# Kernel optimization log

Hardware: AMD Instinct MI355X
Metric: run time of the kernel (lower is better)

Reference implementation:

```python
import jax, jax.numpy as jnp
import numpy as np

LEN = 16384
TAU = 20.0
DT = 1.0


def setup_inputs() -> dict:
    key = jax.random.key(0)
    k1, k2 = jax.random.split(key)
    inp = jax.random.normal(k1, (1024, 1, LEN), dtype=jnp.float32)
    tgt = jax.random.normal(k2, (1024, 1, LEN), dtype=jnp.float32)
    return {"input": inp, "target": tgt}


def _exp_causal_filter(x, decay):
    # x: [B, 1, L]. Causal exponential filter:
    #   y[t] = sum_{m=0}^{t} x[t-m] * decay**m  ==  y[t] = decay*y[t-1] + x[t]
    # This is exactly conv1d(pad(x, (L-1, 0)), kernel=[exp(-t/tau) for t in L-1..0]).
    def step(carry, xt):
        y = decay * carry + xt
        return y, y

    x_t = jnp.moveaxis(x, -1, 0)  # [L, B, 1]
    y0 = jnp.zeros(x.shape[:-1], x.dtype)  # [B, 1]
    _, ys = jax.lax.scan(step, y0, x_t)  # [L, B, 1]
    return jnp.moveaxis(ys, 0, -1)  # [B, 1, L]


def reference(input, target):
    decay = jnp.exp(jnp.asarray(-DT * 0.0 - 1.0 / TAU, input.dtype))  # exp(-1/tau)
    diff = input - target
    filtered = _exp_causal_filter(diff, decay)
    return jnp.sqrt((1.0 / TAU) * jnp.sum(filtered * filtered) * DT)
```

## Files before the change

### kernel.cpp

```cpp
#include <hip/hip_runtime.h>
#include <math.h>

#define LEN       16384
#define NTHREADS  1024
#define SEG       16
#define NWAVES    16

#define DECAY_F 0.951229424500714f
#define D16_F   0.449328964117222f
#define G16_F   7.5886329f

__device__ __forceinline__ int swz(int a) { return a ^ ((a >> 5) & 31); }

#define STEP(xv) { s = __builtin_fmaf(DECAY_F, s, (xv)); ww *= DECAY_F; \
                   A = __builtin_fmaf(s, s, A); Bc = __builtin_fmaf(ww, s, Bc); }

__global__ __launch_bounds__(NTHREADS) void vr_main(
    const float* __restrict__ in, const float* __restrict__ tgt,
    float* __restrict__ partial)
{
    __shared__ float smem[LEN];
    __shared__ float wa[NWAVES], wb[NWAVES], red[NWAVES];

    const int tid  = threadIdx.x;
    const int lane = tid & 63;
    const int wid  = tid >> 6;
    const long long rb = (long long)blockIdx.x * LEN;
    const float4* __restrict__ in4 = (const float4*)(in  + rb);
    const float4* __restrict__ tg4 = (const float4*)(tgt + rb);

    const int cb4 = (wid << 8) + lane;

    const float4 a0 = in4[cb4];       const float4 b0 = tg4[cb4];
    const float4 a1 = in4[cb4 +  64]; const float4 b1 = tg4[cb4 +  64];
    const float4 a2 = in4[cb4 + 128]; const float4 b2 = tg4[cb4 + 128];
    const float4 a3 = in4[cb4 + 192]; const float4 b3 = tg4[cb4 + 192];
    __builtin_amdgcn_sched_barrier(0);

    {
        int base = cb4 * 4;
        smem[swz(base + 0)] = a0.x - b0.x; smem[swz(base + 1)] = a0.y - b0.y;
        smem[swz(base + 2)] = a0.z - b0.z; smem[swz(base + 3)] = a0.w - b0.w;
        base = (cb4 + 64) * 4;
        smem[swz(base + 0)] = a1.x - b1.x; smem[swz(base + 1)] = a1.y - b1.y;
        smem[swz(base + 2)] = a1.z - b1.z; smem[swz(base + 3)] = a1.w - b1.w;
        base = (cb4 + 128) * 4;
        smem[swz(base + 0)] = a2.x - b2.x; smem[swz(base + 1)] = a2.y - b2.y;
        smem[swz(base + 2)] = a2.z - b2.z; smem[swz(base + 3)] = a2.w - b2.w;
        base = (cb4 + 192) * 4;
        smem[swz(base + 0)] = a3.x - b3.x; smem[swz(base + 1)] = a3.y - b3.y;
        smem[swz(base + 2)] = a3.z - b3.z; smem[swz(base + 3)] = a3.w - b3.w;
    }
    asm volatile("s_waitcnt lgkmcnt(0)" ::: "memory");
    __builtin_amdgcn_sched_barrier(0);

    float s = 0.f, A = 0.f, Bc = 0.f, ww = 1.f;
    const int base = tid * SEG;
    #pragma unroll
    for (int i = 0; i < SEG; ++i) {
        const float x = smem[swz(base + i)];
        STEP(x)
    }

    float a = D16_F;
    float b = s;
    #pragma unroll
    for (int j = 1; j < 64; j <<= 1) {
        const float au = __shfl_up(a, j);
        const float bu = __shfl_up(b, j);
        if (lane >= j) {
            b = __builtin_fmaf(a, bu, b);
            a *= au;
        }
    }
    if (lane == 63) { wa[wid] = a; wb[wid] = b; }
    __syncthreads();

    float C = 0.f;
    for (int k = 0; k < wid; ++k) C = __builtin_fmaf(wa[k], C, wb[k]);
    float aex = __shfl_up(a, 1);
    float bex = __shfl_up(b, 1);
    if (lane == 0) { aex = 1.f; bex = 0.f; }
    const float c = __builtin_fmaf(aex, C, bex);

    float part = A + 2.f * c * Bc + (c * c) * G16_F;

    #pragma unroll
    for (int j = 32; j > 0; j >>= 1) part += __shfl_down(part, j);
    if (lane == 0) red[wid] = part;
    __syncthreads();
    if (tid == 0) {
        float t = 0.f;
        #pragma unroll
        for (int k = 0; k < NWAVES; ++k) t += red[k];
        partial[blockIdx.x] = t;
    }
}

__global__ __launch_bounds__(1024) void vr_final(
    const float* __restrict__ partial, int n, float* __restrict__ out)
{
    __shared__ float red[16];
    const int tid = threadIdx.x;
    float v = 0.f;
    for (int k = tid; k < n; k += 1024) v += partial[k];
    #pragma unroll
    for (int j = 32; j > 0; j >>= 1) v += __shfl_down(v, j);
    const int lane = tid & 63, wid = tid >> 6;
    if (lane == 0) red[wid] = v;
    __syncthreads();
    if (tid == 0) {
        float t = 0.f;
        #pragma unroll
        for (int k = 0; k < 16; ++k) t += red[k];
        out[0] = sqrtf(t * 0.05f);
    }
}

extern "C" void kernel_launch(void* const* d_in, const int* in_sizes, int n_in,
                              void* d_out, int out_size, void* d_ws, size_t ws_size,
                              hipStream_t stream) {
    const float* in  = (const float*)d_in[0];
    const float* tgt = (const float*)d_in[1];
    float* out = (float*)d_out;
    float* ws  = (float*)d_ws;
    const int rows = in_sizes[0] / LEN;

    vr_main<<<dim3(rows), dim3(NTHREADS), 0, stream>>>(in, tgt, ws);
    vr_final<<<dim3(1), dim3(1024), 0, stream>>>(ws, rows, out);
}
```

Baseline: 27.95 us.

## Process two rows per block and prefetch the next row during the scan

Each block now handles two rows instead of one. Global loads for the second row are issued right after the first row's differences go to shared memory, so those loads overlap the first row's scan and reduction. This is meant to hide memory latency and cut per-block launch and reduction overhead. The cost is half as many blocks (512 instead of 1024 on 256 CUs), an extra barrier per row, higher register pressure from the prefetched data, and an assumption that the row count is divisible by two.

```diff
diff --git a/kernel.cpp b/kernel.cpp
--- a/kernel.cpp
+++ b/kernel.cpp
@@ -5,6 +5,7 @@
 #define NTHREADS  1024
 #define SEG       16
 #define NWAVES    16
+#define RPB       2
 
 #define DECAY_F 0.951229424500714f
 #define D16_F   0.449328964117222f
@@ -14,6 +15,10 @@
 
 #define STEP(xv) { s = __builtin_fmaf(DECAY_F, s, (xv)); ww *= DECAY_F; \
                    A = __builtin_fmaf(s, s, A); Bc = __builtin_fmaf(ww, s, Bc); }
+
+#define DSW(base4, A4, B4) { const int _b = (base4) * 4; \
+    smem[swz(_b + 0)] = (A4).x - (B4).x; smem[swz(_b + 1)] = (A4).y - (B4).y; \
+    smem[swz(_b + 2)] = (A4).z - (B4).z; smem[swz(_b + 3)] = (A4).w - (B4).w; }
 
 __global__ __launch_bounds__(NTHREADS) void vr_main(
     const float* __restrict__ in, const float* __restrict__ tgt,
@@ -25,69 +30,76 @@
     const int tid  = threadIdx.x;
     const int lane = tid & 63;
     const int wid  = tid >> 6;
-    const long long rb = (long long)blockIdx.x * LEN;
-    const float4* __restrict__ in4 = (const float4*)(in  + rb);
-    const float4* __restrict__ tg4 = (const float4*)(tgt + rb);
-
     const int cb4 = (wid << 8) + lane;
 
-    const float4 a0 = in4[cb4];       const float4 b0 = tg4[cb4];
-    const float4 a1 = in4[cb4 +  64]; const float4 b1 = tg4[cb4 +  64];
-    const float4 a2 = in4[cb4 + 128]; const float4 b2 = tg4[cb4 + 128];
-    const float4 a3 = in4[cb4 + 192]; const float4 b3 = tg4[cb4 + 192];
-    __builtin_amdgcn_sched_barrier(0);
+    const long long row0 = (long long)blockIdx.x * RPB;
+    const float4* __restrict__ in4 = (const float4*)(in  + row0 * LEN);
+    const float4* __restrict__ tg4 = (const float4*)(tgt + row0 * LEN);
 
-    {
-        int base = cb4 * 4;
-        smem[swz(base + 0)] = a0.x - b0.x; smem[swz(base + 1)] = a0.y - b0.y;
-        smem[swz(base + 2)] = a0.z - b0.z; smem[swz(base + 3)] = a0.w - b0.w;
-        base = (cb4 + 64) * 4;
-        smem[swz(base + 0)] = a1.x - b1.x; smem[swz(base + 1)] = a1.y - b1.y;
-        smem[swz(base + 2)] = a1.z - b1.z; smem[swz(base + 3)] = a1.w - b1.w;
-        base = (cb4 + 128) * 4;
-        smem[swz(base + 0)] = a2.x - b2.x; smem[swz(base + 1)] = a2.y - b2.y;
-        smem[swz(base + 2)] = a2.z - b2.z; smem[swz(base + 3)] = a2.w - b2.w;
-        base = (cb4 + 192) * 4;
-        smem[swz(base + 0)] = a3.x - b3.x; smem[swz(base + 1)] = a3.y - b3.y;
-        smem[swz(base + 2)] = a3.z - b3.z; smem[swz(base + 3)] = a3.w - b3.w;
-    }
-    asm volatile("s_waitcnt lgkmcnt(0)" ::: "memory");
-    __builtin_amdgcn_sched_barrier(0);
+    float4 a0 = in4[cb4];       float4 b0 = tg4[cb4];
+    float4 a1 = in4[cb4 +  64]; float4 b1 = tg4[cb4 +  64];
+    float4 a2 = in4[cb4 + 128]; float4 b2 = tg4[cb4 + 128];
+    float4 a3 = in4[cb4 + 192]; float4 b3 = tg4[cb4 + 192];
 
-    float s = 0.f, A = 0.f, Bc = 0.f, ww = 1.f;
-    const int base = tid * SEG;
+    float acc = 0.f;
+
     #pragma unroll
-    for (int i = 0; i < SEG; ++i) {
-        const float x = smem[swz(base + i)];
-        STEP(x)
+    for (int r = 0; r < RPB; ++r) {
+        DSW(cb4,       a0, b0)
+        DSW(cb4 +  64, a1, b1)
+        DSW(cb4 + 128, a2, b2)
+        DSW(cb4 + 192, a3, b3)
+
+        if (r + 1 < RPB) {
+            const float4* __restrict__ i4n =
+                (const float4*)(in  + (row0 + r + 1) * LEN);
+            const float4* __restrict__ t4n =
+                (const float4*)(tgt + (row0 + r + 1) * LEN);
+            a0 = i4n[cb4];       b0 = t4n[cb4];
+            a1 = i4n[cb4 +  64]; b1 = t4n[cb4 +  64];
+            a2 = i4n[cb4 + 128]; b2 = t4n[cb4 + 128];
+            a3 = i4n[cb4 + 192]; b3 = t4n[cb4 + 192];
+        }
+        __builtin_amdgcn_sched_barrier(0);
+        asm volatile("s_waitcnt lgkmcnt(0)" ::: "memory");
+        __builtin_amdgcn_sched_barrier(0);
+
+        float s = 0.f, A = 0.f, Bc = 0.f, ww = 1.f;
+        const int base = tid * SEG;
+        #pragma unroll
+        for (int i = 0; i < SEG; ++i) {
+            const float x = smem[swz(base + i)];
+            STEP(x)
+        }
+
+        float aa = D16_F, bb = s;
+        #pragma unroll
+        for (int j = 1; j < 64; j <<= 1) {
+            const float au = __shfl_up(aa, j);
+            const float bu = __shfl_up(bb, j);
+            if (lane >= j) {
+                bb = __builtin_fmaf(aa, bu, bb);
+                aa *= au;
+            }
+        }
+        if (lane == 63) { wa[wid] = aa; wb[wid] = bb; }
+        __syncthreads();
+
+        float C = 0.f;
+        for (int k = 0; k < wid; ++k) C = __builtin_fmaf(wa[k], C, wb[k]);
+        float aex = __shfl_up(aa, 1);
+        float bex = __shfl_up(bb, 1);
+        if (lane == 0) { aex = 1.f; bex = 0.f; }
+        const float c = __builtin_fmaf(aex, C, bex);
+
+        acc += A + 2.f * c * Bc + (c * c) * G16_F;
+
+        if (r + 1 < RPB) __syncthreads();
     }
 
-    float a = D16_F;
-    float b = s;
     #pragma unroll
-    for (int j = 1; j < 64; j <<= 1) {
-        const float au = __shfl_up(a, j);
-        const float bu = __shfl_up(b, j);
-        if (lane >= j) {
-            b = __builtin_fmaf(a, bu, b);
-            a *= au;
-        }
-    }
-    if (lane == 63) { wa[wid] = a; wb[wid] = b; }
-    __syncthreads();
-
-    float C = 0.f;
-    for (int k = 0; k < wid; ++k) C = __builtin_fmaf(wa[k], C, wb[k]);
-    float aex = __shfl_up(a, 1);
-    float bex = __shfl_up(b, 1);
-    if (lane == 0) { aex = 1.f; bex = 0.f; }
-    const float c = __builtin_fmaf(aex, C, bex);
-
-    float part = A + 2.f * c * Bc + (c * c) * G16_F;
-
-    #pragma unroll
-    for (int j = 32; j > 0; j >>= 1) part += __shfl_down(part, j);
-    if (lane == 0) red[wid] = part;
+    for (int j = 32; j > 0; j >>= 1) acc += __shfl_down(acc, j);
+    if (lane == 0) red[wid] = acc;
     __syncthreads();
     if (tid == 0) {
         float t = 0.f;
@@ -124,8 +136,9 @@
     const float* tgt = (const float*)d_in[1];
     float* out = (float*)d_out;
     float* ws  = (float*)d_ws;
-    const int rows = in_sizes[0] / LEN;
+    const int rows    = in_sizes[0] / LEN;
+    const int nblocks = rows / RPB;
 
-    vr_main<<<dim3(rows), dim3(NTHREADS), 0, stream>>>(in, tgt, ws);
-    vr_final<<<dim3(1), dim3(1024), 0, stream>>>(ws, rows, out);
+    vr_main<<<dim3(nblocks), dim3(NTHREADS), 0, stream>>>(in, tgt, ws);
+    vr_final<<<dim3(1), dim3(1024), 0, stream>>>(ws, nblocks, out);
 }
```

Result: slower. 32.09 us (+14.8%).
